# Optimization experiments

Measured on AMD Instinct MI355X. Metric: run time of the kernel, lower is better.

## Reference

```python
import jax, jax.numpy as jnp
import numpy as np
from jax import lax

NDEMOG, IC, OC, KS = 4, 128, 256, 3
B, H, W = 64, 56, 56


def setup_inputs() -> dict:
    key = jax.random.key(0)
    k1, k2, k3, k4 = jax.random.split(key, 4)
    x = jax.random.normal(k1, (B, IC, H, W), dtype=jnp.float32)
    demog_label = jax.random.randint(k2, (B,), 0, NDEMOG, dtype=jnp.int32)
    kernel_base = jax.random.normal(k3, (OC, IC, KS, KS), dtype=jnp.float32) * 0.05
    kernel_mask = jax.random.uniform(k4, (NDEMOG, IC, KS, KS), dtype=jnp.float32)
    return {"x": x, "demog_label": demog_label, "kernel_base": kernel_base,
            "kernel_mask": kernel_mask, "epoch": 5}


def _conv(x, k):
    # NCHW / OIHW, stride=1, padding=1 (same as F.conv2d(stride=1, padding=1))
    return lax.conv_general_dilated(
        x, k, window_strides=(1, 1), padding=[(1, 1), (1, 1)],
        dimension_numbers=("NCHW", "OIHW", "NCHW"))


def reference(x, demog_label, kernel_base, kernel_mask, epoch):
    # epoch (=5) < fuse_epoch (=9) in the original module, so the per-demographic
    # mask kernel_mask[d] is always used. The torch code gathers the samples of
    # each demographic group, convolves with kernel_base * mask[d], and scatters
    # results back. Equivalent fused form: conv the full batch with each masked
    # kernel and select per-sample by demog_label (ndemog is a small constant).
    ndemog = kernel_mask.shape[0]
    out = jnp.zeros((x.shape[0], kernel_base.shape[0], x.shape[2], x.shape[3]), x.dtype)
    for d in range(ndemog):
        k = kernel_base * kernel_mask[d][None]          # [OC, IC, KS, KS]
        y = _conv(x, k)                                  # [B, OC, H, W]
        sel = (demog_label == d)[:, None, None, None]
        out = out + jnp.where(sel, y, jnp.zeros((), x.dtype))
    return out
```

## Files before the change

### kernel.cpp

```cpp
#include <hip/hip_runtime.h>


typedef __bf16 v8bf __attribute__((ext_vector_type(8)));
typedef float  v4f  __attribute__((ext_vector_type(4)));
typedef unsigned short v8us __attribute__((ext_vector_type(8)));

#define IC_  128
#define OC_  256
#define HH   56
#define WW_  56
#define HW_  3136
#define PW   58
#define XP_PER_B (PW * PW * IC_)
#define WQ_ELEMS (4 * 9 * OC_ * IC_)

__device__ __forceinline__ unsigned short f2bf(float f) {
    unsigned u = __builtin_bit_cast(unsigned, f);
    u += 0x7fffu + ((u >> 16) & 1u);
    return (unsigned short)(u >> 16);
}

typedef __attribute__((address_space(3))) unsigned int lds_u32_t;
typedef const __attribute__((address_space(1))) unsigned int gbl_u32_t;

__device__ __forceinline__ void gload_lds16(const unsigned short* gsrc, unsigned short* ldst) {
    __builtin_amdgcn_global_load_lds((gbl_u32_t*)gsrc,
                                     (lds_u32_t*)(unsigned int)(unsigned long long)(uintptr_t)ldst,
                                     16, 0, 0);
}

__global__ __launch_bounds__(256)
void transpose_pad(const float* __restrict__ x, unsigned short* __restrict__ xp)
{
    __shared__ unsigned short lt[IC_ * 58];
    const int blk = blockIdx.x;
    const int b = blk / HH, h = blk % HH;
    const int t = threadIdx.x;
    const float* xb = x + (size_t)b * IC_ * HW_ + h * WW_;
    #pragma unroll
    for (int i = 0; i < 7; ++i) {
        int e4 = t + i * 256;
        int ic = e4 / 14;
        int w4 = (e4 - ic * 14) * 4;
        v4f v = *(const v4f*)&xb[ic * HW_ + w4];
        unsigned lo = (unsigned)f2bf(v[0]) | ((unsigned)f2bf(v[1]) << 16);
        unsigned hi = (unsigned)f2bf(v[2]) | ((unsigned)f2bf(v[3]) << 16);
        unsigned* dst = (unsigned*)&lt[ic * 58 + w4];
        dst[0] = lo;
        dst[1] = hi;
    }
    __syncthreads();
    unsigned short* xpb = xp + (size_t)b * XP_PER_B + (size_t)(h + 1) * PW * IC_;
    #pragma unroll
    for (int i = 0; i < 4; ++i) {
        int s = t + i * 256;
        if (s < 896) {
            int w = s >> 4, icg = s & 15;
            unsigned short v[8];
            #pragma unroll
            for (int j = 0; j < 8; ++j) v[j] = lt[(icg * 8 + j) * 58 + w];
            *(v8us*)&xpb[(w + 1) * IC_ + icg * 8] = *(const v8us*)v;
        }
    }
    if (t < 32) {
        int col = (t >> 4) * 57;
        *(v8us*)&xpb[(size_t)col * IC_ + (t & 15) * 8] = (v8us)(unsigned short)0;
    }
    if (h == 0 || h == HH - 1) {
        unsigned short* row = xp + (size_t)b * XP_PER_B + (h == 0 ? 0 : (size_t)(PW - 1) * PW * IC_);
        for (int s = t; s < 928; s += 256)
            *(v8us*)&row[(size_t)s * 8] = (v8us)(unsigned short)0;
    }
}

__global__ __launch_bounds__(256)
void build_weights(const float* __restrict__ kbase, const float* __restrict__ kmask,
                   unsigned short* __restrict__ wq)
{
    int t  = blockIdx.x * 256 + threadIdx.x;
    int ic = t & 127;
    int oc = (t >> 7) & 255;
    int rd = t >> 15;
    int r  = rd % 9, d = rd / 9;
    float v = kbase[oc * 1152 + ic * 9 + r] * kmask[d * 1152 + ic * 9 + r];
    wq[t] = f2bf(v);
}

__global__ __launch_bounds__(256, 2)
void adaconv_main(const unsigned short* __restrict__ xp,
                  const unsigned short* __restrict__ wq,
                  const int* __restrict__ demog,
                  float* __restrict__ out)
{
    __shared__ unsigned short panel[232 * 64];
    __shared__ unsigned short bbuf[3][256 * 32];

    const int t    = threadIdx.x;
    const int lane = t & 63;
    const int quad = lane >> 4;
    const int l15  = lane & 15;
    const int wid  = __builtin_amdgcn_readfirstlane(t >> 6);

    const int lin = blockIdx.y * 49 + blockIdx.x;
    const int nl  = (lin & 7) * 392 + (lin >> 3);
    const int mtile = nl % 49;
    const int b     = nl / 49;

    const int p0 = mtile * 64;
    const int d  = demog[b];
    const int h0 = p0 / WW_;

    int baseR[4];
    #pragma unroll
    for (int mi = 0; mi < 4; ++mi) {
        int pix = p0 + mi * 16 + l15;
        int hh  = pix / WW_;
        int wwp = pix - hh * WW_;
        baseR[mi] = (hh - h0 + 1) * PW + (wwp + 1);
    }

    const int olane = ((lane >> 3) << 7) + (((lane & 7) ^ (lane >> 3)) << 3);
    const unsigned short* xpb = xp + (size_t)b * XP_PER_B + (size_t)h0 * PW * IC_;

    const int slotp = (lane & 7) ^ (lane >> 3);
    const int ocb   = 2 * (wid * 8 + (lane >> 3)) + (slotp >> 2);
    const unsigned short* sB = wq + (size_t)d * 9 * OC_ * IC_
                             + (size_t)ocb * IC_ + (slotp & 3) * 8;

    int bOff[4];
    #pragma unroll
    for (int ni = 0; ni < 4; ++ni) {
        int oc = wid * 64 + ni * 16 + l15;
        int r128 = oc >> 1;
        bOff[ni] = (r128 << 7) + (((((oc & 1) << 2) | quad) ^ (r128 & 7)) << 4);
    }

    v4f acc[4][4];
    #pragma unroll
    for (int mi = 0; mi < 4; ++mi)
        #pragma unroll
        for (int ni = 0; ni < 4; ++ni)
            acc[mi][ni] = (v4f)0.0f;

    int tA[4];

    #define STAGEA(half_) do {                                                  \
        const unsigned short* xph_ = xpb + (half_) * 64;                        \
        _Pragma("unroll")                                                       \
        for (int kk = 0; kk < 8; ++kk) {                                        \
            int k_ = wid + kk * 4;                                              \
            if (k_ < 29) gload_lds16(xph_ + k_ * 1024 + olane, panel + k_ * 512); \
        } } while (0)

    #define STAGEB(bufi, c_) do {                                               \
        const int r_   = ((c_) % 18) >> 1;                                      \
        const int ic0_ = ((c_) / 18) * 64 + (((c_) % 18) & 1) * 32;             \
        const unsigned short* s_ = sB + r_ * (OC_ * IC_) + ic0_;                \
        _Pragma("unroll")                                                       \
        for (int j = 0; j < 4; ++j)                                             \
            gload_lds16(s_ + j * 64 * IC_, &bbuf[bufi][wid * 512 + j * 2048]);  \
        } while (0)

    #define SETTAP(r_) do {                                                     \
        const int offR_ = ((r_) / 3 - 1) * PW + ((r_) % 3 - 1);                 \
        _Pragma("unroll")                                                       \
        for (int mi = 0; mi < 4; ++mi) {                                        \
            int R_ = baseR[mi] + offR_;                                         \
            tA[mi] = (R_ << 7) + (((R_ & 7) ^ quad) << 4);                      \
        } } while (0)

    STAGEA(0);
    STAGEB(0, 0);
    STAGEB(1, 1);
    asm volatile("s_waitcnt vmcnt(0)" ::: "memory");
    __builtin_amdgcn_s_barrier();

    #pragma unroll
    for (int c = 0; c < 36; ++c) {
        if (c > 0) {
            if (c < 35) asm volatile("s_waitcnt vmcnt(4)" ::: "memory");
            else        asm volatile("s_waitcnt vmcnt(0)" ::: "memory");
            __builtin_amdgcn_s_barrier();
        }
        if (c == 18) STAGEA(1);
        if (c + 2 < 36) STAGEB((c + 2) % 3, c + 2);
        if (c == 18) asm volatile("s_waitcnt vmcnt(4)" ::: "memory");

        const int r   = (c % 18) >> 1;
        const int icb = (c % 18) & 1;
        if (icb == 0) SETTAP(r);

        v8us au[4], bu[4];
        #pragma unroll
        for (int mi = 0; mi < 4; ++mi)
            au[mi] = *(const v8us*)((const char*)panel + (tA[mi] ^ (icb << 6)));
        #pragma unroll
        for (int ni = 0; ni < 4; ++ni)
            bu[ni] = *(const v8us*)((const char*)bbuf[c % 3] + bOff[ni]);

        __builtin_amdgcn_s_setprio(1);
        #pragma unroll
        for (int mi = 0; mi < 4; ++mi) {
            v8bf a = __builtin_bit_cast(v8bf, au[mi]);
            #pragma unroll
            for (int ni = 0; ni < 4; ++ni) {
                v8bf bb = __builtin_bit_cast(v8bf, bu[ni]);
                acc[mi][ni] = __builtin_amdgcn_mfma_f32_16x16x32_bf16(a, bb, acc[mi][ni], 0, 0, 0);
            }
        }
        __builtin_amdgcn_s_setprio(0);
    }
    #undef STAGEA
    #undef STAGEB
    #undef SETTAP

    float* ob = out + ((size_t)b * OC_ + wid * 64) * HW_ + p0;
    #pragma unroll
    for (int ni = 0; ni < 4; ++ni) {
        #pragma unroll
        for (int mi = 0; mi < 4; ++mi) {
            float* o = ob + (size_t)(ni * 16 + l15) * HW_ + mi * 16 + quad * 4;
            *(v4f*)o = acc[mi][ni];
        }
    }
}

extern "C" void kernel_launch(void* const* d_in, const int* in_sizes, int n_in,
                              void* d_out, int out_size, void* d_ws, size_t ws_size,
                              hipStream_t stream) {
    const float* x     = (const float*)d_in[0];
    const int*   demog = (const int*)d_in[1];
    const float* kbase = (const float*)d_in[2];
    const float* kmask = (const float*)d_in[3];
    float* out = (float*)d_out;

    unsigned short* xp = (unsigned short*)d_ws;
    unsigned short* wq = xp + (size_t)64 * XP_PER_B;
    transpose_pad<<<64 * HH, 256, 0, stream>>>(x, xp);
    build_weights<<<WQ_ELEMS / 256, 256, 0, stream>>>(kbase, kmask, wq);
    adaconv_main<<<dim3(49, 64), 256, 0, stream>>>(xp, wq, demog, out);
}
```

Measured before the change: 420.6 us.

## Software-pipeline LDS fragment reads with double-buffered registers ahead of MFMAs

Restructures the main K loop so the LDS reads of the A and B fragments for the next step go into a second register set while the current step's MFMAs issue, instead of reading and then computing serially. The per-wave B staging layout is also remapped so each wave loads its own contiguous 64 output channels. The mid-loop switch to the second input-channel half is handled with a dedicated barrier and full wait. This costs more VGPRs, which may reduce occupancy, and it shifts where the barriers sit around the triple-buffered B tiles.

```diff
diff --git a/kernel.cpp b/kernel.cpp
--- a/kernel.cpp
+++ b/kernel.cpp
@@ -123,9 +123,9 @@
     const unsigned short* xpb = xp + (size_t)b * XP_PER_B + (size_t)h0 * PW * IC_;
 
     const int slotp = (lane & 7) ^ (lane >> 3);
-    const int ocb   = 2 * (wid * 8 + (lane >> 3)) + (slotp >> 2);
     const unsigned short* sB = wq + (size_t)d * 9 * OC_ * IC_
-                             + (size_t)ocb * IC_ + (slotp & 3) * 8;
+                             + (size_t)(64 * wid + 2 * (lane >> 3) + (slotp >> 2)) * IC_
+                             + (slotp & 3) * 8;
 
     int bOff[4];
     #pragma unroll
@@ -142,7 +142,8 @@
         for (int ni = 0; ni < 4; ++ni)
             acc[mi][ni] = (v4f)0.0f;
 
-    int tA[4];
+    int  tA[4];
+    v8us au[2][4], bu[2][4];
 
     #define STAGEA(half_) do {                                                  \
         const unsigned short* xph_ = xpb + (half_) * 64;                        \
@@ -152,13 +153,12 @@
             if (k_ < 29) gload_lds16(xph_ + k_ * 1024 + olane, panel + k_ * 512); \
         } } while (0)
 
-    #define STAGEB(bufi, c_) do {                                               \
-        const int r_   = ((c_) % 18) >> 1;                                      \
-        const int ic0_ = ((c_) / 18) * 64 + (((c_) % 18) & 1) * 32;             \
-        const unsigned short* s_ = sB + r_ * (OC_ * IC_) + ic0_;                \
+    #define STAGEB(bufi_, cc_) do {                                             \
+        const int cl_  = (cc_) % 18;                                            \
+        const int off_ = (cl_ >> 1) * (OC_ * IC_) + ((cc_) / 18) * 64 + (cl_ & 1) * 32; \
         _Pragma("unroll")                                                       \
         for (int j = 0; j < 4; ++j)                                             \
-            gload_lds16(s_ + j * 64 * IC_, &bbuf[bufi][wid * 512 + j * 2048]);  \
+            gload_lds16(sB + off_ + j * 16 * IC_, &bbuf[bufi_][wid * 2048 + j * 512]); \
         } while (0)
 
     #define SETTAP(r_) do {                                                     \
@@ -169,50 +169,68 @@
             tA[mi] = (R_ << 7) + (((R_ & 7) ^ quad) << 4);                      \
         } } while (0)
 
+    #define READA(set_, cc_) do {                                               \
+        const int cl_ = (cc_) % 18;                                             \
+        if ((cl_ & 1) == 0) SETTAP(cl_ >> 1);                                   \
+        _Pragma("unroll")                                                       \
+        for (int mi = 0; mi < 4; ++mi)                                          \
+            au[set_][mi] = *(const v8us*)((const char*)panel + (tA[mi] ^ ((cl_ & 1) << 6))); \
+        } while (0)
+
+    #define READB(set_, cc_) do {                                               \
+        _Pragma("unroll")                                                       \
+        for (int ni = 0; ni < 4; ++ni)                                          \
+            bu[set_][ni] = *(const v8us*)((const char*)bbuf[(cc_) % 3] + bOff[ni]); \
+        } while (0)
+
+    #define DOMFMA(set_) do {                                                   \
+        __builtin_amdgcn_s_setprio(1);                                          \
+        _Pragma("unroll")                                                       \
+        for (int mi = 0; mi < 4; ++mi) {                                        \
+            v8bf a_ = __builtin_bit_cast(v8bf, au[set_][mi]);                   \
+            _Pragma("unroll")                                                   \
+            for (int ni = 0; ni < 4; ++ni) {                                    \
+                v8bf b_ = __builtin_bit_cast(v8bf, bu[set_][ni]);               \
+                acc[mi][ni] = __builtin_amdgcn_mfma_f32_16x16x32_bf16(a_, b_, acc[mi][ni], 0, 0, 0); \
+            }                                                                   \
+        }                                                                       \
+        __builtin_amdgcn_s_setprio(0);                                          \
+    } while (0)
+
     STAGEA(0);
+    asm volatile("" ::: "memory");
     STAGEB(0, 0);
     STAGEB(1, 1);
     asm volatile("s_waitcnt vmcnt(0)" ::: "memory");
     __builtin_amdgcn_s_barrier();
+    READA(0, 0);
+    READB(0, 0);
 
     #pragma unroll
     for (int c = 0; c < 36; ++c) {
-        if (c > 0) {
-            if (c < 35) asm volatile("s_waitcnt vmcnt(4)" ::: "memory");
-            else        asm volatile("s_waitcnt vmcnt(0)" ::: "memory");
+        DOMFMA(c & 1);
+        if (c == 17) {
+            STAGEB(1, 19);
             __builtin_amdgcn_s_barrier();
+            STAGEA(1);
+            asm volatile("s_waitcnt vmcnt(0)" ::: "memory");
+            __builtin_amdgcn_s_barrier();
+            READA(0, 18);
+            READB(0, 18);
+        } else if (c < 35) {
+            if (c + 2 < 36) STAGEB((c + 2) % 3, c + 2);
+            READA((c + 1) & 1, c + 1);
+            if (c + 2 < 36) asm volatile("s_waitcnt vmcnt(4)" ::: "memory");
+            else            asm volatile("s_waitcnt vmcnt(0)" ::: "memory");
+            READB((c + 1) & 1, c + 1);
         }
-        if (c == 18) STAGEA(1);
-        if (c + 2 < 36) STAGEB((c + 2) % 3, c + 2);
-        if (c == 18) asm volatile("s_waitcnt vmcnt(4)" ::: "memory");
-
-        const int r   = (c % 18) >> 1;
-        const int icb = (c % 18) & 1;
-        if (icb == 0) SETTAP(r);
-
-        v8us au[4], bu[4];
-        #pragma unroll
-        for (int mi = 0; mi < 4; ++mi)
-            au[mi] = *(const v8us*)((const char*)panel + (tA[mi] ^ (icb << 6)));
-        #pragma unroll
-        for (int ni = 0; ni < 4; ++ni)
-            bu[ni] = *(const v8us*)((const char*)bbuf[c % 3] + bOff[ni]);
-
-        __builtin_amdgcn_s_setprio(1);
-        #pragma unroll
-        for (int mi = 0; mi < 4; ++mi) {
-            v8bf a = __builtin_bit_cast(v8bf, au[mi]);
-            #pragma unroll
-            for (int ni = 0; ni < 4; ++ni) {
-                v8bf bb = __builtin_bit_cast(v8bf, bu[ni]);
-                acc[mi][ni] = __builtin_amdgcn_mfma_f32_16x16x32_bf16(a, bb, acc[mi][ni], 0, 0, 0);
-            }
-        }
-        __builtin_amdgcn_s_setprio(0);
     }
     #undef STAGEA
     #undef STAGEB
     #undef SETTAP
+    #undef READA
+    #undef READB
+    #undef DOMFMA
 
     float* ob = out + ((size_t)b * OC_ + wid * 64) * HW_ + p0;
     #pragma unroll
```

After: 417.3 us. Within noise of the previous version (-0.8%).
